# Kernel tuning notes

Measured on AMD Instinct MI355X. Metric: run time of the kernel, lower is better.

The kernel has to match this reference:

```python
import jax, jax.numpy as jnp
import numpy as np

E, IN, H1, H2, H3, A, B = 20, 512, 1024, 512, 256, 32, 4096


def setup_inputs() -> dict:
    key = jax.random.key(0)
    ks = jax.random.split(key, 10)

    def w(k, shape, fan_in):
        return jax.random.normal(k, shape, dtype=jnp.float32) / np.sqrt(fan_in)

    return {
        "obs": jax.random.normal(ks[0], (B, IN), dtype=jnp.float32),
        # stacked expert MLP params [E, ...]
        "eW1": w(ks[1], (E, IN, H1), IN), "eb1": jnp.zeros((E, H1), jnp.float32),
        "eW2": w(ks[2], (E, H1, H2), H1), "eb2": jnp.zeros((E, H2), jnp.float32),
        "eW3": w(ks[3], (E, H2, H3), H2), "eb3": jnp.zeros((E, H3), jnp.float32),
        "eW4": w(ks[4], (E, H3, A), H3), "eb4": jnp.zeros((E, A), jnp.float32),
        # gate MLP params
        "gW1": w(ks[5], (IN, H1), IN), "gb1": jnp.zeros((H1,), jnp.float32),
        "gW2": w(ks[6], (H1, H2), H1), "gb2": jnp.zeros((H2,), jnp.float32),
        "gW3": w(ks[7], (H2, H3), H2), "gb3": jnp.zeros((H3,), jnp.float32),
        "gW4": w(ks[8], (H3, E), H3), "gb4": jnp.zeros((E,), jnp.float32),
    }


def _experts(obs, eW1, eb1, eW2, eb2, eW3, eb3, eW4, eb4):
    # batched over experts: [B, E, h]
    h = jax.nn.elu(jnp.einsum('bi,eih->beh', obs, eW1) + eb1[None])
    h = jax.nn.elu(jnp.einsum('beh,ehk->bek', h, eW2) + eb2[None])
    h = jax.nn.elu(jnp.einsum('bek,ekm->bem', h, eW3) + eb3[None])
    return jnp.einsum('bem,ema->bea', h, eW4) + eb4[None]  # [B, E, A]


def _gate(obs, gW1, gb1, gW2, gb2, gW3, gb3, gW4, gb4):
    h = jax.nn.elu(obs @ gW1 + gb1)
    h = jax.nn.elu(h @ gW2 + gb2)
    h = jax.nn.elu(h @ gW3 + gb3)
    return jax.nn.softmax(h @ gW4 + gb4, axis=-1)  # [B, E]


def reference(obs, eW1, eb1, eW2, eb2, eW3, eb3, eW4, eb4,
              gW1, gb1, gW2, gb2, gW3, gb3, gW4, gb4):
    weights = _gate(obs, gW1, gb1, gW2, gb2, gW3, gb3, gW4, gb4)       # [B, E]
    actions = _experts(obs, eW1, eb1, eW2, eb2, eW3, eb3, eW4, eb4)    # [B, E, A]
    # bmm(weights[:,None,:], actions).squeeze(1)
    return jnp.einsum('be,bea->ba', weights, actions)                   # [B, A]
```

## Files before the change

kernel.cpp:

```cpp
#include <hip/hip_runtime.h>

#define B_SZ 4096
#define E_EXP 20
#define NE 21

typedef unsigned short u16;
typedef __bf16 bf16x8 __attribute__((ext_vector_type(8)));
typedef u16 u16x8 __attribute__((ext_vector_type(8)));
typedef u16 u16x4 __attribute__((ext_vector_type(4)));
typedef float floatx4 __attribute__((ext_vector_type(4)));

static __device__ __forceinline__ u16 f2bf(float f) {
  unsigned u = __builtin_bit_cast(unsigned, f);
  u += 0x7fffu + ((u >> 16) & 1u);
  return (u16)(u >> 16);
}

static __device__ __forceinline__ float elu1(float v) {
  return v > 0.f ? v : (__expf(v) - 1.f);
}

static __device__ __forceinline__ bf16x8 ld_bf8(const u16* p) {
  u16x8 v = *reinterpret_cast<const u16x8*>(p);
  return __builtin_bit_cast(bf16x8, v);
}

static __device__ __forceinline__ void gld_lds16(const u16* g, u16* l) {
  __builtin_amdgcn_global_load_lds(
      (const __attribute__((address_space(1))) unsigned int*)g,
      (__attribute__((address_space(3))) unsigned int*)l, 16, 0, 0);
}


__global__ void prep_small_kernel(
    const float* __restrict__ obs, u16* __restrict__ obs_bf,
    const float* __restrict__ eb1, const float* __restrict__ gb1,
    const float* __restrict__ eb2, const float* __restrict__ gb2,
    const float* __restrict__ eb3, const float* __restrict__ gb3,
    float* __restrict__ b1, float* __restrict__ b2, float* __restrict__ b3) {
  int bid = blockIdx.x;
  if (bid < 2048) {
    int i = (bid * 256 + threadIdx.x) * 4;
    float4 v = *reinterpret_cast<const float4*>(obs + i);
    u16x4 o;
    o.x = f2bf(v.x); o.y = f2bf(v.y); o.z = f2bf(v.z); o.w = f2bf(v.w);
    *reinterpret_cast<u16x4*>(obs_bf + i) = o;
  } else {
    int i = (bid - 2048) * 256 + threadIdx.x;
    const int S1 = NE * 1024, S2 = NE * 512, S3 = NE * 256;
    if (i < S1) {
      b1[i] = (i < E_EXP * 1024) ? eb1[i] : gb1[i - E_EXP * 1024];
    } else if (i < S1 + S2) {
      int j = i - S1;
      b2[j] = (j < E_EXP * 512) ? eb2[j] : gb2[j - E_EXP * 512];
    } else if (i < S1 + S2 + S3) {
      int j = i - S1 - S2;
      b3[j] = (j < E_EXP * 256) ? eb3[j] : gb3[j - E_EXP * 256];
    }
  }
}

#define TRANS_BLOCKS 6132

__global__ __launch_bounds__(256) void transpose_all_kernel(
    const float* __restrict__ eW1, const float* __restrict__ gW1,
    const float* __restrict__ eW2, const float* __restrict__ gW2,
    const float* __restrict__ eW3, const float* __restrict__ gW3,
    const float* __restrict__ eW4, const float* __restrict__ gW4,
    u16* __restrict__ W1t, u16* __restrict__ W2t, u16* __restrict__ W3t,
    u16* __restrict__ W4t, u16* __restrict__ gW4t) {
  int f = blockIdx.x;
  const float *srcE, *srcG;
  u16* dstBase;
  int rem, K, N, Nout, kxt, tpm, nm;
  if (f < 2688) {
    rem = f;        srcE = eW1; srcG = gW1; dstBase = W1t;
    K = 512;  N = 1024; Nout = 1024; kxt = 8;  tpm = 128; nm = 20;
  } else if (f < 5376) {
    rem = f - 2688; srcE = eW2; srcG = gW2; dstBase = W2t;
    K = 1024; N = 512;  Nout = 512;  kxt = 16; tpm = 128; nm = 20;
  } else if (f < 6048) {
    rem = f - 5376; srcE = eW3; srcG = gW3; dstBase = W3t;
    K = 512;  N = 256;  Nout = 256;  kxt = 8;  tpm = 32;  nm = 20;
  } else if (f < 6128) {
    rem = f - 6048; srcE = eW4; srcG = nullptr; dstBase = W4t;
    K = 256;  N = 32;   Nout = 32;   kxt = 4;  tpm = 4;   nm = 99;
  } else {
    rem = f - 6128; srcE = gW4; srcG = nullptr; dstBase = gW4t;
    K = 256;  N = 20;   Nout = 32;   kxt = 4;  tpm = 4;   nm = 99;
  }
  int mat = rem / tpm;
  int t = rem % tpm;
  const float* src = (mat < nm) ? (srcE + (long)mat * K * N) : srcG;
  u16* dst = dstBase + (long)mat * Nout * K;
  int kbase = (t % kxt) * 64;
  int nbase = (t / kxt) * 64;

  __shared__ float tl[64][65];
  int tid = threadIdx.x;
  int kk = tid >> 4;
  int n4 = (tid & 15) * 4;
#pragma unroll
  for (int p = 0; p < 4; ++p) {
    int k = kbase + p * 16 + kk;
    int n = nbase + n4;
    float4 v = make_float4(0.f, 0.f, 0.f, 0.f);
    if (n + 3 < N) {
      v = *reinterpret_cast<const float4*>(&src[(long)k * N + n]);
    } else {
      float* vp = &v.x;
      for (int j = 0; j < 4; ++j)
        if (n + j < N) vp[j] = src[(long)k * N + n + j];
    }
    tl[p * 16 + kk][n4 + 0] = v.x;
    tl[p * 16 + kk][n4 + 1] = v.y;
    tl[p * 16 + kk][n4 + 2] = v.z;
    tl[p * 16 + kk][n4 + 3] = v.w;
  }
  __syncthreads();

  int kk8 = (tid & 7) * 8;
#pragma unroll
  for (int p = 0; p < 2; ++p) {
    int ln = p * 32 + (tid >> 3);
    int n = nbase + ln;
    if (n < Nout) {
      u16x8 o;
#pragma unroll
      for (int j = 0; j < 8; ++j) o[j] = f2bf(tl[kk8 + j][ln]);
      *reinterpret_cast<u16x8*>(&dst[(long)n * K + kbase + kk8]) = o;
    }
  }
}


#define BM 128
#define BN 128

__global__ __launch_bounds__(256) void gemm_bias_elu_kernel(
    const u16* __restrict__ A_base, long a_estride,
    const u16* __restrict__ Wt_base, long w_estride,
    const float* __restrict__ bias_base, long b_estride,
    u16* __restrict__ C_base, long c_estride,
    int M, int N, int K, int ntn, int ntm) {
  int per = gridDim.x >> 3;
  int wid = (blockIdx.x & 7) * per + (blockIdx.x >> 3);
  int tpe = ntn * ntm;
  int e = wid / tpe;
  int rem = wid - e * tpe;
  int mt = rem / ntn;
  int nt = rem - mt * ntn;
  int m0 = mt * BM;
  int n0 = nt * BN;

  const u16* A = A_base + (long)e * a_estride;
  const u16* Wt = Wt_base + (long)e * w_estride;
  const float* bias = bias_base + (long)e * b_estride;
  u16* C = C_base + (long)e * c_estride;

  __shared__ u16 As[2 * BM * 32];
  __shared__ u16 Bs[2 * BN * 32];

  int tid = threadIdx.x;
  int lane = tid & 63;
  int w = tid >> 6;
  int wm = (w >> 1) * 64;
  int wn = (w & 1) * 64;
  int col = lane & 15;
  int quad = lane >> 4;

  floatx4 acc[4][4] = {};

  int srow = tid >> 2;
  int scol = (tid & 3) * 8;
  const u16* gA = &A[(long)(m0 + srow) * K + scol];
  const u16* gB = &Wt[(long)(n0 + srow) * K + scol];
  long rowK = (long)64 * K;

  for (int k0 = 0; k0 < K; k0 += 64) {
    __syncthreads();
    gld_lds16(gA + k0, &As[(size_t)tid * 8]);
    gld_lds16(gA + rowK + k0, &As[(size_t)(256 + tid) * 8]);
    gld_lds16(gA + k0 + 32, &As[(size_t)(512 + tid) * 8]);
    gld_lds16(gA + rowK + k0 + 32, &As[(size_t)(768 + tid) * 8]);
    gld_lds16(gB + k0, &Bs[(size_t)tid * 8]);
    gld_lds16(gB + rowK + k0, &Bs[(size_t)(256 + tid) * 8]);
    gld_lds16(gB + k0 + 32, &Bs[(size_t)(512 + tid) * 8]);
    gld_lds16(gB + rowK + k0 + 32, &Bs[(size_t)(768 + tid) * 8]);
    __syncthreads();

#pragma unroll
    for (int kk = 0; kk < 2; ++kk) {
      bf16x8 xf[4], wf[4];
#pragma unroll
      for (int t = 0; t < 4; ++t) {
        xf[t] = __builtin_bit_cast(bf16x8,
            *reinterpret_cast<u16x8*>(
                &As[kk * BM * 32 + (wm + t * 16 + col) * 32 + quad * 8]));
        wf[t] = __builtin_bit_cast(bf16x8,
            *reinterpret_cast<u16x8*>(
                &Bs[kk * BN * 32 + (wn + t * 16 + col) * 32 + quad * 8]));
      }
#pragma unroll
      for (int i = 0; i < 4; ++i)
#pragma unroll
        for (int j = 0; j < 4; ++j)
          acc[i][j] = __builtin_amdgcn_mfma_f32_16x16x32_bf16(
              wf[j], xf[i], acc[i][j], 0, 0, 0);
    }
  }

#pragma unroll
  for (int j = 0; j < 4; ++j) {
    int nn = n0 + wn + j * 16 + quad * 4;
    float4 b4 = *reinterpret_cast<const float4*>(&bias[nn]);
#pragma unroll
    for (int i = 0; i < 4; ++i) {
      int m = m0 + wm + i * 16 + col;
      u16x4 o;
      o.x = f2bf(elu1(acc[i][j][0] + b4.x));
      o.y = f2bf(elu1(acc[i][j][1] + b4.y));
      o.z = f2bf(elu1(acc[i][j][2] + b4.z));
      o.w = f2bf(elu1(acc[i][j][3] + b4.w));
      *reinterpret_cast<u16x4*>(&C[(long)m * N + nn]) = o;
    }
  }
}

__global__ __launch_bounds__(256) void final_combine_kernel(
    const u16* __restrict__ h3, const u16* __restrict__ W4t,
    const u16* __restrict__ gW4t, const float* __restrict__ eb4,
    const float* __restrict__ gb4, float* __restrict__ out) {
  const int H3 = 256;
  int tid = threadIdx.x;
  int lane = tid & 63;
  int w = tid >> 6;
  int col = lane & 15;
  int quad = lane >> 4;
  int r0 = blockIdx.x * 16;

  floatx4 g0 = {}, g1 = {};
  const u16* h3g = h3 + (long)E_EXP * B_SZ * H3;
#pragma unroll
  for (int k0 = 0; k0 < 256; k0 += 32) {
    bf16x8 a = ld_bf8(&h3g[(long)(r0 + col) * H3 + k0 + quad * 8]);
    bf16x8 b0 = ld_bf8(&gW4t[(long)col * H3 + k0 + quad * 8]);
    bf16x8 b1 = ld_bf8(&gW4t[(long)(16 + col) * H3 + k0 + quad * 8]);
    g0 = __builtin_amdgcn_mfma_f32_16x16x32_bf16(a, b0, g0, 0, 0, 0);
    g1 = __builtin_amdgcn_mfma_f32_16x16x32_bf16(a, b1, g1, 0, 0, 0);
  }

  float w0[4], w1[4];
  float gbc0 = gb4[col];
  float gbc1 = (col < 4) ? gb4[16 + col] : 0.f;
#pragma unroll
  for (int r = 0; r < 4; ++r) {
    float v0 = g0[r] + gbc0;
    float v1 = (col < 4) ? (g1[r] + gbc1) : -1e30f;
    float m = fmaxf(v0, v1);
#pragma unroll
    for (int s = 1; s < 16; s <<= 1) m = fmaxf(m, __shfl_xor(m, s, 64));
    float e0 = __expf(v0 - m);
    float e1 = (col < 4) ? __expf(v1 - m) : 0.f;
    float ssum = e0 + e1;
#pragma unroll
    for (int s = 1; s < 16; s <<= 1) ssum += __shfl_xor(ssum, s, 64);
    w0[r] = e0 / ssum;
    w1[r] = e1 / ssum;
  }

  floatx4 o0 = {}, o1 = {};
  for (int e = w; e < E_EXP; e += 4) {
    floatx4 a0 = {}, a1 = {};
    const u16* he = h3 + (long)e * B_SZ * H3;
    const u16* we = W4t + (long)e * 32 * H3;
#pragma unroll
    for (int k0 = 0; k0 < 256; k0 += 32) {
      bf16x8 a = ld_bf8(&he[(long)(r0 + col) * H3 + k0 + quad * 8]);
      bf16x8 b0 = ld_bf8(&we[(long)col * H3 + k0 + quad * 8]);
      bf16x8 b1 = ld_bf8(&we[(long)(16 + col) * H3 + k0 + quad * 8]);
      a0 = __builtin_amdgcn_mfma_f32_16x16x32_bf16(a, b0, a0, 0, 0, 0);
      a1 = __builtin_amdgcn_mfma_f32_16x16x32_bf16(a, b1, a1, 0, 0, 0);
    }
    float be0 = eb4[e * 32 + col];
    float be1 = eb4[e * 32 + 16 + col];
    int src = (lane & 48) + (e & 15);
#pragma unroll
    for (int r = 0; r < 4; ++r) {
      float wr = __shfl((e < 16) ? w0[r] : w1[r], src, 64);
      o0[r] += wr * (a0[r] + be0);
      o1[r] += wr * (a1[r] + be1);
    }
  }

  __shared__ float red[3][64][8];
  if (w > 0) {
#pragma unroll
    for (int r = 0; r < 4; ++r) {
      red[w - 1][lane][r] = o0[r];
      red[w - 1][lane][4 + r] = o1[r];
    }
  }
  __syncthreads();
  if (w == 0) {
#pragma unroll
    for (int ww = 0; ww < 3; ++ww)
#pragma unroll
      for (int r = 0; r < 4; ++r) {
        o0[r] += red[ww][lane][r];
        o1[r] += red[ww][lane][4 + r];
      }
#pragma unroll
    for (int r = 0; r < 4; ++r) {
      int row = r0 + quad * 4 + r;
      out[(long)row * 32 + col] = o0[r];
      out[(long)row * 32 + 16 + col] = o1[r];
    }
  }
}


static inline size_t align256(size_t x) { return (x + 255) & ~(size_t)255; }

extern "C" void kernel_launch(void* const* d_in, const int* in_sizes, int n_in,
                              void* d_out, int out_size, void* d_ws,
                              size_t ws_size, hipStream_t stream) {
  const float* obs = (const float*)d_in[0];
  const float* eW1 = (const float*)d_in[1];
  const float* eb1 = (const float*)d_in[2];
  const float* eW2 = (const float*)d_in[3];
  const float* eb2 = (const float*)d_in[4];
  const float* eW3 = (const float*)d_in[5];
  const float* eb3 = (const float*)d_in[6];
  const float* eW4 = (const float*)d_in[7];
  const float* eb4 = (const float*)d_in[8];
  const float* gW1 = (const float*)d_in[9];
  const float* gb1 = (const float*)d_in[10];
  const float* gW2 = (const float*)d_in[11];
  const float* gb2 = (const float*)d_in[12];
  const float* gW3 = (const float*)d_in[13];
  const float* gb3 = (const float*)d_in[14];
  const float* gW4 = (const float*)d_in[15];
  const float* gb4 = (const float*)d_in[16];
  float* out = (float*)d_out;
  char* ws = (char*)d_ws;

  size_t off = 0;
  size_t OFF_OBS = off;  off = align256(off + (size_t)B_SZ * 512 * 2);
  size_t OFF_W1T = off;  off = align256(off + (size_t)NE * 1024 * 512 * 2);
  size_t OFF_W2T = off;  off = align256(off + (size_t)NE * 512 * 1024 * 2);
  size_t OFF_W3T = off;  off = align256(off + (size_t)NE * 256 * 512 * 2);
  size_t OFF_W4T = off;  off = align256(off + (size_t)E_EXP * 32 * 256 * 2);
  size_t OFF_GW4T = off; off = align256(off + (size_t)32 * 256 * 2);
  size_t OFF_B1 = off;   off = align256(off + (size_t)NE * 1024 * 4);
  size_t OFF_B2 = off;   off = align256(off + (size_t)NE * 512 * 4);
  size_t OFF_B3 = off;   off = align256(off + (size_t)NE * 256 * 4);
  size_t OFF_H3 = off;   off = align256(off + (size_t)NE * B_SZ * 256 * 2);

  int chunk = B_SZ;
  size_t OFF_H1 = off;
  while (chunk > 512) {
    size_t need = (size_t)NE * chunk * 1024 * 2 + (size_t)NE * chunk * 512 * 2;
    if (OFF_H1 + need <= ws_size) break;
    chunk >>= 1;
  }
  size_t OFF_H2 = align256(OFF_H1 + (size_t)NE * chunk * 1024 * 2);

  u16* obs_bf = (u16*)(ws + OFF_OBS);
  u16* W1t = (u16*)(ws + OFF_W1T);
  u16* W2t = (u16*)(ws + OFF_W2T);
  u16* W3t = (u16*)(ws + OFF_W3T);
  u16* W4t = (u16*)(ws + OFF_W4T);
  u16* gW4t = (u16*)(ws + OFF_GW4T);
  float* b1 = (float*)(ws + OFF_B1);
  float* b2 = (float*)(ws + OFF_B2);
  float* b3 = (float*)(ws + OFF_B3);
  u16* h3 = (u16*)(ws + OFF_H3);
  u16* h1 = (u16*)(ws + OFF_H1);
  u16* h2 = (u16*)(ws + OFF_H2);

  prep_small_kernel<<<2048 + (NE * 1792 + 255) / 256, 256, 0, stream>>>(
      obs, obs_bf, eb1, gb1, eb2, gb2, eb3, gb3, b1, b2, b3);
  transpose_all_kernel<<<TRANS_BLOCKS, 256, 0, stream>>>(
      eW1, gW1, eW2, gW2, eW3, gW3, eW4, gW4, W1t, W2t, W3t, W4t, gW4t);

  int ntm = chunk / BM;
  for (int bc = 0; bc < B_SZ; bc += chunk) {
    gemm_bias_elu_kernel<<<NE * 8 * ntm, 256, 0, stream>>>(
        obs_bf + (size_t)bc * 512, 0L,
        W1t, (long)1024 * 512,
        b1, 1024L,
        h1, (long)chunk * 1024, chunk, 1024, 512, 8, ntm);
    gemm_bias_elu_kernel<<<NE * 4 * ntm, 256, 0, stream>>>(
        h1, (long)chunk * 1024,
        W2t, (long)512 * 1024,
        b2, 512L,
        h2, (long)chunk * 512, chunk, 512, 1024, 4, ntm);
    gemm_bias_elu_kernel<<<NE * 2 * ntm, 256, 0, stream>>>(
        h2, (long)chunk * 512,
        W3t, (long)256 * 512,
        b3, 256L,
        h3 + (size_t)bc * 256, (long)B_SZ * 256, chunk, 256, 512, 2, ntm);
  }

  final_combine_kernel<<<B_SZ / 16, 256, 0, stream>>>(h3, W4t, gW4t, eb4, gb4,
                                                      out);
}
```

Baseline: 495.3 us.

## Rewrite expert GEMM as 256x256 tiles with swizzled LDS and two-stage prefetch

The bias+ELU GEMM grows from 128x128 to 256x256 tiles with 512 threads and 128 KB of LDS. It also gains an XOR-swizzled shared layout to avoid bank conflicts and a double-buffered pipeline that issues global-to-LDS loads two k-steps ahead between MFMA phases. The aim is more operand reuse per LDS byte and overlap of memory latency with matrix math. In exchange it launches fewer workgroups, which risks under-filling the CUs for the smaller layer-3 GEMM, and its correctness depends on hand-placed waitcnt and barrier counts. The XCD remap is also made robust to grid sizes that are not multiples of 8.

```diff
diff --git a/kernel.cpp b/kernel.cpp
--- a/kernel.cpp
+++ b/kernel.cpp
@@ -134,17 +134,21 @@
 }
 
 
-#define BM 128
-#define BN 128
-
-__global__ __launch_bounds__(256) void gemm_bias_elu_kernel(
+#define BM 256
+#define BN 256
+
+__global__ __launch_bounds__(512) void gemm_bias_elu_kernel(
     const u16* __restrict__ A_base, long a_estride,
     const u16* __restrict__ Wt_base, long w_estride,
     const float* __restrict__ bias_base, long b_estride,
     u16* __restrict__ C_base, long c_estride,
     int M, int N, int K, int ntn, int ntm) {
-  int per = gridDim.x >> 3;
-  int wid = (blockIdx.x & 7) * per + (blockIdx.x >> 3);
+  int nwg = gridDim.x;
+  int orig = blockIdx.x;
+  int xcd = orig & 7;
+  int q8 = nwg >> 3, r8 = nwg & 7;
+  int wid = (xcd < r8 ? xcd * (q8 + 1) : r8 * (q8 + 1) + (xcd - r8) * q8) +
+            (orig >> 3);
   int tpe = ntn * ntm;
   int e = wid / tpe;
   int rem = wid - e * tpe;
@@ -158,65 +162,117 @@
   const float* bias = bias_base + (long)e * b_estride;
   u16* C = C_base + (long)e * c_estride;
 
-  __shared__ u16 As[2 * BM * 32];
-  __shared__ u16 Bs[2 * BN * 32];
+  __shared__ __align__(16) unsigned char smem[131072];
 
   int tid = threadIdx.x;
   int lane = tid & 63;
   int w = tid >> 6;
-  int wm = (w >> 1) * 64;
-  int wn = (w & 1) * 64;
+  int wm = w >> 2;
+  int wn = w & 3;
   int col = lane & 15;
   int quad = lane >> 4;
 
-  floatx4 acc[4][4] = {};
-
-  int srow = tid >> 2;
-  int scol = (tid & 3) * 8;
-  const u16* gA = &A[(long)(m0 + srow) * K + scol];
-  const u16* gB = &Wt[(long)(n0 + srow) * K + scol];
-  long rowK = (long)64 * K;
-
-  for (int k0 = 0; k0 < K; k0 += 64) {
-    __syncthreads();
-    gld_lds16(gA + k0, &As[(size_t)tid * 8]);
-    gld_lds16(gA + rowK + k0, &As[(size_t)(256 + tid) * 8]);
-    gld_lds16(gA + k0 + 32, &As[(size_t)(512 + tid) * 8]);
-    gld_lds16(gA + rowK + k0 + 32, &As[(size_t)(768 + tid) * 8]);
-    gld_lds16(gB + k0, &Bs[(size_t)tid * 8]);
-    gld_lds16(gB + rowK + k0, &Bs[(size_t)(256 + tid) * 8]);
-    gld_lds16(gB + k0 + 32, &Bs[(size_t)(512 + tid) * 8]);
-    gld_lds16(gB + rowK + k0 + 32, &Bs[(size_t)(768 + tid) * 8]);
-    __syncthreads();
-
-#pragma unroll
-    for (int kk = 0; kk < 2; ++kk) {
-      bf16x8 xf[4], wf[4];
-#pragma unroll
-      for (int t = 0; t < 4; ++t) {
-        xf[t] = __builtin_bit_cast(bf16x8,
-            *reinterpret_cast<u16x8*>(
-                &As[kk * BM * 32 + (wm + t * 16 + col) * 32 + quad * 8]));
-        wf[t] = __builtin_bit_cast(bf16x8,
-            *reinterpret_cast<u16x8*>(
-                &Bs[kk * BN * 32 + (wn + t * 16 + col) * 32 + quad * 8]));
+  int sLog = (tid & 7) ^ ((tid >> 3) & 7);
+  int rA0 = ((tid >> 3) & 31) + ((tid & 256) ? 128 : 0);
+  const u16* gA = A + (long)(m0 + rA0) * K + sLog * 8;
+  const u16* gB = Wt + (long)(n0 + (tid >> 3)) * K + sLog * 8;
+  int dstOff = tid * 16;
+
+  int xo0 = (quad ^ (col & 7)) * 16;
+  int aBase = (wm * 32 + col) * 128;
+  int bBase = (wn * 64 + col) * 128;
+
+  floatx4 acc[8][4] = {};
+  bf16x8 bf[4][2];
+  int NT = K >> 6;
+
+  auto stageA = [&](int b, int q, int k0) {
+    gld_lds16(gA + (long)(q * 32) * K + k0,
+              (u16*)(smem + b * 65536 + q * 8192 + dstOff));
+  };
+  auto stageB = [&](int b, int i, int k0) {
+    gld_lds16(gB + (long)(i * 64) * K + k0,
+              (u16*)(smem + b * 65536 + 32768 + i * 8192 + dstOff));
+  };
+  auto ldA = [&](int b, int q, int f, int kk) -> bf16x8 {
+    return ld_bf8((const u16*)(smem + b * 65536 + q * 8192 + aBase +
+                               f * 2048 + (xo0 ^ (kk * 64))));
+  };
+  auto ldB = [&](int b, int j, int kk) -> bf16x8 {
+    return ld_bf8((const u16*)(smem + b * 65536 + 32768 + bBase + j * 2048 +
+                               (xo0 ^ (kk * 64))));
+  };
+
+  stageB(0, 0, 0); stageB(0, 1, 0); stageB(0, 2, 0); stageB(0, 3, 0);
+  stageA(0, 0, 0); stageA(0, 1, 0); stageA(0, 2, 0); stageA(0, 3, 0);
+  if (NT > 1) {
+    stageB(1, 0, 64); stageB(1, 1, 64); stageB(1, 2, 64); stageB(1, 3, 64);
+    stageA(1, 0, 64); stageA(1, 1, 64);
+    asm volatile("s_waitcnt vmcnt(6)" ::: "memory");
+  } else {
+    asm volatile("s_waitcnt vmcnt(0)" ::: "memory");
+  }
+  __builtin_amdgcn_s_barrier();
+
+  for (int t = 0; t < NT; ++t) {
+    int b = t & 1;
+    int nb = b ^ 1;
+    int kc1 = (t + 1) << 6;
+    int kc2 = (t + 2) << 6;
+    bool s1 = (t + 1 < NT);
+    bool s2 = (t + 2 < NT);
+
+#pragma unroll
+    for (int q = 0; q < 4; ++q) {
+      bf16x8 a00 = ldA(b, q, 0, 0);
+      bf16x8 a01 = ldA(b, q, 0, 1);
+      bf16x8 a10 = ldA(b, q, 1, 0);
+      bf16x8 a11 = ldA(b, q, 1, 1);
+      if (q == 0) {
+#pragma unroll
+        for (int j = 0; j < 4; ++j) {
+          bf[j][0] = ldB(b, j, 0);
+          bf[j][1] = ldB(b, j, 1);
+        }
+        if (s1) { stageA(nb, 2, kc1); stageA(nb, 3, kc1); }
+      } else if (q == 1) {
+        if (s2) { stageB(b, 0, kc2); stageB(b, 1, kc2); }
+      } else if (q == 2) {
+        if (s2) { stageB(b, 2, kc2); stageB(b, 3, kc2); }
+      } else {
+        if (s2) { stageA(b, 0, kc2); stageA(b, 1, kc2); }
       }
-#pragma unroll
-      for (int i = 0; i < 4; ++i)
-#pragma unroll
-        for (int j = 0; j < 4; ++j)
-          acc[i][j] = __builtin_amdgcn_mfma_f32_16x16x32_bf16(
-              wf[j], xf[i], acc[i][j], 0, 0, 0);
+      __builtin_amdgcn_s_barrier();
+      asm volatile("s_waitcnt lgkmcnt(0)" ::: "memory");
+      __builtin_amdgcn_sched_barrier(0);
+      __builtin_amdgcn_s_setprio(1);
+#pragma unroll
+      for (int j = 0; j < 4; ++j) {
+        acc[2 * q][j] = __builtin_amdgcn_mfma_f32_16x16x32_bf16(
+            bf[j][0], a00, acc[2 * q][j], 0, 0, 0);
+        acc[2 * q][j] = __builtin_amdgcn_mfma_f32_16x16x32_bf16(
+            bf[j][1], a01, acc[2 * q][j], 0, 0, 0);
+        acc[2 * q + 1][j] = __builtin_amdgcn_mfma_f32_16x16x32_bf16(
+            bf[j][0], a10, acc[2 * q + 1][j], 0, 0, 0);
+        acc[2 * q + 1][j] = __builtin_amdgcn_mfma_f32_16x16x32_bf16(
+            bf[j][1], a11, acc[2 * q + 1][j], 0, 0, 0);
+      }
+      __builtin_amdgcn_s_setprio(0);
+      if (q == 3 && s1) {
+        if (s2) asm volatile("s_waitcnt vmcnt(6)" ::: "memory");
+        else    asm volatile("s_waitcnt vmcnt(0)" ::: "memory");
+      }
+      __builtin_amdgcn_s_barrier();
     }
   }
 
 #pragma unroll
   for (int j = 0; j < 4; ++j) {
-    int nn = n0 + wn + j * 16 + quad * 4;
+    int nn = n0 + wn * 64 + j * 16 + quad * 4;
     float4 b4 = *reinterpret_cast<const float4*>(&bias[nn]);
 #pragma unroll
-    for (int i = 0; i < 4; ++i) {
-      int m = m0 + wm + i * 16 + col;
+    for (int i = 0; i < 8; ++i) {
+      int m = m0 + wm * 128 + i * 16 + col;
       u16x4 o;
       o.x = f2bf(elu1(acc[i][j][0] + b4.x));
       o.y = f2bf(elu1(acc[i][j][1] + b4.y));
@@ -386,21 +442,21 @@
 
   int ntm = chunk / BM;
   for (int bc = 0; bc < B_SZ; bc += chunk) {
-    gemm_bias_elu_kernel<<<NE * 8 * ntm, 256, 0, stream>>>(
+    gemm_bias_elu_kernel<<<NE * 4 * ntm, 512, 0, stream>>>(
         obs_bf + (size_t)bc * 512, 0L,
         W1t, (long)1024 * 512,
         b1, 1024L,
-        h1, (long)chunk * 1024, chunk, 1024, 512, 8, ntm);
-    gemm_bias_elu_kernel<<<NE * 4 * ntm, 256, 0, stream>>>(
+        h1, (long)chunk * 1024, chunk, 1024, 512, 4, ntm);
+    gemm_bias_elu_kernel<<<NE * 2 * ntm, 512, 0, stream>>>(
         h1, (long)chunk * 1024,
         W2t, (long)512 * 1024,
         b2, 512L,
-        h2, (long)chunk * 512, chunk, 512, 1024, 4, ntm);
-    gemm_bias_elu_kernel<<<NE * 2 * ntm, 256, 0, stream>>>(
+        h2, (long)chunk * 512, chunk, 512, 1024, 2, ntm);
+    gemm_bias_elu_kernel<<<NE * 1 * ntm, 512, 0, stream>>>(
         h2, (long)chunk * 512,
         W3t, (long)256 * 512,
         b3, 256L,
-        h3 + (size_t)bc * 256, (long)B_SZ * 256, chunk, 256, 512, 2, ntm);
+        h3 + (size_t)bc * 256, (long)B_SZ * 256, chunk, 256, 512, 1, ntm);
   }
 
   final_combine_kernel<<<B_SZ / 16, 256, 0, stream>>>(h3, W4t, gW4t, eb4, gb4,
```

Result: slower. 527.9 us (+6.6%).

## Load MFMA fragments directly from global memory and halve the N tile

Applied to the files above, without the earlier changes.

Replaces the LDS-staged double tile loads with per-wave direct global vector loads of A and W fragments into registers, removing all __syncthreads barriers from the K loop. The N tile shrinks from 128 to 64 with a 4-blocks-per-CU launch bound, and the grids double to match. The intent is to cut LDS and barrier overhead and raise occupancy, but data reuse across waves now depends on caches, so global and L2 traffic rise.

```diff
diff --git a/kernel.cpp b/kernel.cpp
--- a/kernel.cpp
+++ b/kernel.cpp
@@ -23,12 +23,6 @@
 static __device__ __forceinline__ bf16x8 ld_bf8(const u16* p) {
   u16x8 v = *reinterpret_cast<const u16x8*>(p);
   return __builtin_bit_cast(bf16x8, v);
-}
-
-static __device__ __forceinline__ void gld_lds16(const u16* g, u16* l) {
-  __builtin_amdgcn_global_load_lds(
-      (const __attribute__((address_space(1))) unsigned int*)g,
-      (__attribute__((address_space(3))) unsigned int*)l, 16, 0, 0);
 }
 
 
@@ -135,9 +129,9 @@
 
 
 #define BM 128
-#define BN 128
-
-__global__ __launch_bounds__(256) void gemm_bias_elu_kernel(
+#define BN 64
+
+__global__ __launch_bounds__(256, 4) void gemm_bias_elu_kernel(
     const u16* __restrict__ A_base, long a_estride,
     const u16* __restrict__ Wt_base, long w_estride,
     const float* __restrict__ bias_base, long b_estride,
@@ -158,70 +152,55 @@
   const float* bias = bias_base + (long)e * b_estride;
   u16* C = C_base + (long)e * c_estride;
 
-  __shared__ u16 As[2 * BM * 32];
-  __shared__ u16 Bs[2 * BN * 32];
-
   int tid = threadIdx.x;
   int lane = tid & 63;
   int w = tid >> 6;
   int wm = (w >> 1) * 64;
-  int wn = (w & 1) * 64;
+  int wn = (w & 1) * 32;
   int col = lane & 15;
   int quad = lane >> 4;
 
-  floatx4 acc[4][4] = {};
-
-  int srow = tid >> 2;
-  int scol = (tid & 3) * 8;
-  const u16* gA = &A[(long)(m0 + srow) * K + scol];
-  const u16* gB = &Wt[(long)(n0 + srow) * K + scol];
-  long rowK = (long)64 * K;
-
+  floatx4 acc[4][2] = {};
+
+  const u16* a0 = &A[(long)(m0 + wm + col) * K + quad * 8];
+  const u16* b0 = &Wt[(long)(n0 + wn + col) * K + quad * 8];
+  long r16 = (long)16 * K;
+
+#pragma unroll 2
   for (int k0 = 0; k0 < K; k0 += 64) {
-    __syncthreads();
-    gld_lds16(gA + k0, &As[(size_t)tid * 8]);
-    gld_lds16(gA + rowK + k0, &As[(size_t)(256 + tid) * 8]);
-    gld_lds16(gA + k0 + 32, &As[(size_t)(512 + tid) * 8]);
-    gld_lds16(gA + rowK + k0 + 32, &As[(size_t)(768 + tid) * 8]);
-    gld_lds16(gB + k0, &Bs[(size_t)tid * 8]);
-    gld_lds16(gB + rowK + k0, &Bs[(size_t)(256 + tid) * 8]);
-    gld_lds16(gB + k0 + 32, &Bs[(size_t)(512 + tid) * 8]);
-    gld_lds16(gB + rowK + k0 + 32, &Bs[(size_t)(768 + tid) * 8]);
-    __syncthreads();
-
 #pragma unroll
     for (int kk = 0; kk < 2; ++kk) {
-      bf16x8 xf[4], wf[4];
-#pragma unroll
-      for (int t = 0; t < 4; ++t) {
-        xf[t] = __builtin_bit_cast(bf16x8,
-            *reinterpret_cast<u16x8*>(
-                &As[kk * BM * 32 + (wm + t * 16 + col) * 32 + quad * 8]));
-        wf[t] = __builtin_bit_cast(bf16x8,
-            *reinterpret_cast<u16x8*>(
-                &Bs[kk * BN * 32 + (wn + t * 16 + col) * 32 + quad * 8]));
-      }
+      int ko = k0 + kk * 32;
+      bf16x8 xf[4], wf[2];
+#pragma unroll
+      for (int t4 = 0; t4 < 4; ++t4) xf[t4] = ld_bf8(a0 + t4 * r16 + ko);
+#pragma unroll
+      for (int j = 0; j < 2; ++j) wf[j] = ld_bf8(b0 + j * r16 + ko);
 #pragma unroll
       for (int i = 0; i < 4; ++i)
 #pragma unroll
-        for (int j = 0; j < 4; ++j)
+        for (int j = 0; j < 2; ++j)
           acc[i][j] = __builtin_amdgcn_mfma_f32_16x16x32_bf16(
               wf[j], xf[i], acc[i][j], 0, 0, 0);
     }
   }
 
-#pragma unroll
-  for (int j = 0; j < 4; ++j) {
-    int nn = n0 + wn + j * 16 + quad * 4;
-    float4 b4 = *reinterpret_cast<const float4*>(&bias[nn]);
-#pragma unroll
-    for (int i = 0; i < 4; ++i) {
-      int m = m0 + wm + i * 16 + col;
+  float4 b4[2];
+#pragma unroll
+  for (int j = 0; j < 2; ++j)
+    b4[j] = *reinterpret_cast<const float4*>(
+        &bias[n0 + wn + j * 16 + quad * 4]);
+#pragma unroll
+  for (int i = 0; i < 4; ++i) {
+    int m = m0 + wm + i * 16 + col;
+#pragma unroll
+    for (int j = 0; j < 2; ++j) {
+      int nn = n0 + wn + j * 16 + quad * 4;
       u16x4 o;
-      o.x = f2bf(elu1(acc[i][j][0] + b4.x));
-      o.y = f2bf(elu1(acc[i][j][1] + b4.y));
-      o.z = f2bf(elu1(acc[i][j][2] + b4.z));
-      o.w = f2bf(elu1(acc[i][j][3] + b4.w));
+      o.x = f2bf(elu1(acc[i][j][0] + b4[j].x));
+      o.y = f2bf(elu1(acc[i][j][1] + b4[j].y));
+      o.z = f2bf(elu1(acc[i][j][2] + b4[j].z));
+      o.w = f2bf(elu1(acc[i][j][3] + b4[j].w));
       *reinterpret_cast<u16x4*>(&C[(long)m * N + nn]) = o;
     }
   }
@@ -386,21 +365,21 @@
 
   int ntm = chunk / BM;
   for (int bc = 0; bc < B_SZ; bc += chunk) {
-    gemm_bias_elu_kernel<<<NE * 8 * ntm, 256, 0, stream>>>(
+    gemm_bias_elu_kernel<<<NE * 16 * ntm, 256, 0, stream>>>(
         obs_bf + (size_t)bc * 512, 0L,
         W1t, (long)1024 * 512,
         b1, 1024L,
-        h1, (long)chunk * 1024, chunk, 1024, 512, 8, ntm);
-    gemm_bias_elu_kernel<<<NE * 4 * ntm, 256, 0, stream>>>(
+        h1, (long)chunk * 1024, chunk, 1024, 512, 16, ntm);
+    gemm_bias_elu_kernel<<<NE * 8 * ntm, 256, 0, stream>>>(
         h1, (long)chunk * 1024,
         W2t, (long)512 * 1024,
         b2, 512L,
-        h2, (long)chunk * 512, chunk, 512, 1024, 4, ntm);
-    gemm_bias_elu_kernel<<<NE * 2 * ntm, 256, 0, stream>>>(
+        h2, (long)chunk * 512, chunk, 512, 1024, 8, ntm);
+    gemm_bias_elu_kernel<<<NE * 4 * ntm, 256, 0, stream>>>(
         h2, (long)chunk * 512,
         W3t, (long)256 * 512,
         b3, 256L,
-        h3 + (size_t)bc * 256, (long)B_SZ * 256, chunk, 256, 512, 2, ntm);
+        h3 + (size_t)bc * 256, (long)B_SZ * 256, chunk, 256, 512, 4, ntm);
   }
 
   final_combine_kernel<<<B_SZ / 16, 256, 0, stream>>>(h3, W4t, gW4t, eb4, gb4,
```

Result: slower. 1.292 ms (+160.8%).
